# Kernel tuning notes

Measured on AMD Instinct MI355X. Metric: run time of the kernel, lower is better.

Reference implementation:

```python
import jax, jax.numpy as jnp
import numpy as np

H = 16      # num_attention_heads
D = 64      # attention_head_size
HID = H * D # hidden_size = 1024
N = 1024    # seq_len == max_len
K = 1024    # position_buckets == att_span (K >= N so un-clamped indices stay in range)
EPS = 1e-7  # layer_norm_eps


def setup_inputs() -> dict:
    key = jax.random.key(0)
    ks = jax.random.split(key, 12)

    def w(k, shape):
        return jax.random.normal(k, shape, dtype=jnp.float32) * 0.02

    return {
        "hidden_states": jax.random.normal(ks[0], (1, N, HID), dtype=jnp.float32),
        "rel_embeddings": jax.random.normal(ks[1], (2 * K, HID), dtype=jnp.float32),
        "Wq": w(ks[2], (HID, HID)), "bq": jnp.zeros((HID,), jnp.float32),
        "Wk": w(ks[3], (HID, HID)), "bk": jnp.zeros((HID,), jnp.float32),
        "Wv": w(ks[4], (HID, HID)), "bv": jnp.zeros((HID,), jnp.float32),
        "Wpk": w(ks[5], (HID, HID)), "bpk": jnp.zeros((HID,), jnp.float32),
        "Wpq": w(ks[6], (HID, HID)), "bpq": jnp.zeros((HID,), jnp.float32),
        "Wo": w(ks[7], (HID, HID)), "bo": jnp.zeros((HID,), jnp.float32),
        "ln_g": jnp.ones((HID,), jnp.float32),
        "ln_b": jnp.zeros((HID,), jnp.float32),
    }


def _heads(x):
    # (L, HID) -> (H, L, D)   (batch size is 1, matching the baked-in id offsets)
    L = x.shape[0]
    return x.reshape(L, H, D).transpose(1, 0, 2)


def reference(hidden_states, rel_embeddings, Wq, bq, Wk, bk, Wv, bv,
              Wpk, bpk, Wpq, bpq, Wo, bo, ln_g, ln_b):
    hs = hidden_states[0]                       # (N, HID)
    q = _heads(hs @ Wq.T + bq)                  # (H, N, D)
    k = _heads(hs @ Wk.T + bk)                  # (H, N, D)
    v = _heads(hs @ Wv.T + bv)                  # (H, N, D)

    scale = jnp.sqrt(jnp.asarray(D * 3, jnp.float32))  # scale_factor = 1 + c2p + p2c = 3
    scores = jnp.einsum('hid,hjd->hij', q, k) / scale  # (H, N, N)

    pos_k = _heads(rel_embeddings @ Wpk.T + bpk)       # (H, 2K, D)
    pos_q = _heads(rel_embeddings @ Wpq.T + bpq)       # (H, 2K, D)

    rows = jnp.arange(N)[:, None]                      # (N, 1)
    # ids[i, j] = (i - j) + K  (no clamp in the original; valid since K >= N)
    idx = K + jnp.arange(N)[:, None] - jnp.arange(N)[None, :]  # (N, N)

    # c2p: gather c2p_att[h, i, K + i - j]
    c2p_att = jnp.einsum('hid,hkd->hik', q, pos_k)     # (H, N, 2K)
    c2p = c2p_att[:, rows, idx]                        # (H, N, N)

    # p2c: gather p2c_att[h, i, K + j - i], then transpose last two dims
    p2c_att = jnp.einsum('hid,hkd->hik', k, pos_q)     # (H, N, 2K)
    p2c = jnp.swapaxes(p2c_att[:, rows, idx.T], -1, -2)  # (H, N, N)

    scores = scores + (c2p + p2c) / scale
    attn = jax.nn.softmax(scores, axis=-1)             # (H, N, N)

    ctx = jnp.einsum('hij,hjd->hid', attn, v)          # (H, N, D)
    ctx = ctx.transpose(1, 0, 2).reshape(1, N, HID)    # (1, N, HID)

    # DebertaV2SelfOutput: dense + residual LayerNorm
    out = ctx @ Wo.T + bo
    x = out + hidden_states
    mu = jnp.mean(x, axis=-1, keepdims=True)
    var = jnp.mean(jnp.square(x - mu), axis=-1, keepdims=True)
    return ((x - mu) / jnp.sqrt(var + EPS)) * ln_g + ln_b
```

## Files before the change

### kernel.cpp

```cpp
#include <hip/hip_runtime.h>
#include <stdint.h>

#define HID 1024
#define NSEQ 1024
#define KREL 1024
#define NHEAD 16
#define DHEAD 64

typedef __attribute__((ext_vector_type(8))) short bhalf8;
typedef __attribute__((ext_vector_type(4))) float floatx4;

__device__ inline uint16_t f2bf(float f) {
  union { float f; uint32_t u; } c; c.f = f;
  uint32_t u = c.u;
  return (uint16_t)((u + 0x7fffu + ((u >> 16) & 1u)) >> 16);
}
__device__ inline uint32_t pkbf(float a, float b) {
  union { float f; uint32_t u; } x, y; x.f = a; y.f = b;
#if __has_builtin(__builtin_amdgcn_perm)
  return __builtin_amdgcn_perm(x.u + 0x8000u, y.u + 0x8000u, 0x03020706u);
#else
  return ((x.u + 0x8000u) >> 16) | ((y.u + 0x8000u) & 0xffff0000u);
#endif
}

struct Cast8 {
  const float* src[8];
  uint16_t* dst[8];
  int n[8];
};
__global__ __launch_bounds__(256) void cast8_kernel(Cast8 c) {
  int seg = blockIdx.y;
  int n = c.n[seg];
  const float* s = c.src[seg];
  uint16_t* d = c.dst[seg];
  for (int idx = (blockIdx.x * 256 + threadIdx.x) * 4; idx < n; idx += 1024 * 256 * 4) {
    float4 v = *(const float4*)(s + idx);
    ushort4 o;
    o.x = f2bf(v.x); o.y = f2bf(v.y); o.z = f2bf(v.z); o.w = f2bf(v.w);
    *(ushort4*)(d + idx) = o;
  }
}

struct ProjArgs {
  const uint16_t* A[5];
  const uint16_t* W[5];
  const float* bias[5];
  uint16_t* C[5];
  int trans[5];
};
__global__ __launch_bounds__(256) void proj_gemm(ProjArgs pa) {
  __shared__ uint16_t a_s[2][128 * 40];
  __shared__ uint16_t b_s[2][128 * 40];
  int bidx = blockIdx.x;
  int xcd = bidx & 7, idx = bidx >> 3;
  int g = xcd * 7 + (idx >> 3);
  int nt = idx & 7;
  int z, mt;
  if (g < 24) { z = g >> 3; mt = g & 7; }
  else { int g2 = g - 24; z = 3 + (g2 >> 4); mt = g2 & 15; }
  const uint16_t* A = pa.A[z];
  const uint16_t* W = pa.W[z];
  int i0 = mt * 128, n0 = nt * 128;

  int t = threadIdx.x;
  int lane = t & 63, w = t >> 6;
  int fm = lane & 15, kq = lane >> 4;
  int wm = (w >> 1) * 64, wn = (w & 1) * 64;

  int ra = t >> 1, ca = (t & 1) * 16;
  const uint16_t* Ap = A + (size_t)(i0 + ra) * HID + ca;
  const uint16_t* Wp = W + (size_t)(n0 + ra) * HID + ca;

  floatx4 acc[4][4] = {};

  uint4 ua0 = *(const uint4*)(Ap);
  uint4 ua1 = *(const uint4*)(Ap + 8);
  uint4 ub0 = *(const uint4*)(Wp);
  uint4 ub1 = *(const uint4*)(Wp + 8);
  *(uint4*)(&a_s[0][ra * 40 + ca]) = ua0;
  *(uint4*)(&a_s[0][ra * 40 + ca + 8]) = ua1;
  *(uint4*)(&b_s[0][ra * 40 + ca]) = ub0;
  *(uint4*)(&b_s[0][ra * 40 + ca + 8]) = ub1;

  for (int kt = 0; kt < 32; ++kt) {
    __syncthreads();
    int cur = kt & 1;
    if (kt < 31) {
      int ko = (kt + 1) * 32;
      ua0 = *(const uint4*)(Ap + ko);
      ua1 = *(const uint4*)(Ap + ko + 8);
      ub0 = *(const uint4*)(Wp + ko);
      ub1 = *(const uint4*)(Wp + ko + 8);
    }
    const uint16_t* as = &a_s[cur][0];
    const uint16_t* bs = &b_s[cur][0];
    bhalf8 af[4], bf[4];
#pragma unroll
    for (int m2 = 0; m2 < 4; ++m2)
      af[m2] = *(bhalf8*)(as + (wm + m2 * 16 + fm) * 40 + kq * 8);
#pragma unroll
    for (int n2 = 0; n2 < 4; ++n2)
      bf[n2] = *(bhalf8*)(bs + (wn + n2 * 16 + fm) * 40 + kq * 8);
#pragma unroll
    for (int m2 = 0; m2 < 4; ++m2)
#pragma unroll
      for (int n2 = 0; n2 < 4; ++n2)
        acc[m2][n2] = __builtin_amdgcn_mfma_f32_16x16x32_bf16(af[m2], bf[n2], acc[m2][n2], 0, 0, 0);
    if (kt < 31) {
      int nxt = cur ^ 1;
      *(uint4*)(&a_s[nxt][ra * 40 + ca]) = ua0;
      *(uint4*)(&a_s[nxt][ra * 40 + ca + 8]) = ua1;
      *(uint4*)(&b_s[nxt][ra * 40 + ca]) = ub0;
      *(uint4*)(&b_s[nxt][ra * 40 + ca + 8]) = ub1;
    }
  }

  const float* bias = pa.bias[z];
  uint16_t* C = pa.C[z];
  int tr = pa.trans[z];
#pragma unroll
  for (int m2 = 0; m2 < 4; ++m2) {
    int rowb = i0 + wm + m2 * 16 + kq * 4;
#pragma unroll
    for (int n2 = 0; n2 < 4; ++n2) {
      int col = n0 + wn + n2 * 16 + fm;
      float bv = bias[col];
      floatx4 v = acc[m2][n2];
      if (tr) {
        uint2 p = { pkbf(v[0] + bv, v[1] + bv), pkbf(v[2] + bv, v[3] + bv) };
        *(uint2*)(C + (size_t)col * NSEQ + rowb) = p;
      } else {
#pragma unroll
        for (int r = 0; r < 4; ++r)
          C[(size_t)(rowb + r) * HID + col] = f2bf(v[r] + bv);
      }
    }
  }
}

__global__ __launch_bounds__(256) void out_gemm(const uint16_t* __restrict__ Abf,
                                                const uint16_t* __restrict__ W,
                                                const float* __restrict__ bias,
                                                float* __restrict__ C) {
  __shared__ uint16_t a_s[2][64 * 40];
  __shared__ uint16_t b_s[2][64 * 40];
  int bidx = blockIdx.x;
  int i0 = (bidx >> 4) * 64, n0 = (bidx & 15) * 64;
  int t = threadIdx.x;
  int lane = t & 63, w = t >> 6;
  int fm = lane & 15, kq = lane >> 4;
  int wm = (w >> 1) * 32, wn = (w & 1) * 32;
  int ra = t >> 2, ca = (t & 3) * 8;
  const uint16_t* Ap = Abf + (size_t)(i0 + ra) * HID + ca;
  const uint16_t* Wp = W + (size_t)(n0 + ra) * HID + ca;
  floatx4 acc00 = {0,0,0,0}, acc01 = {0,0,0,0}, acc10 = {0,0,0,0}, acc11 = {0,0,0,0};
  uint4 ua = *(const uint4*)(Ap);
  uint4 ub = *(const uint4*)(Wp);
  *(uint4*)(&a_s[0][ra * 40 + ca]) = ua;
  *(uint4*)(&b_s[0][ra * 40 + ca]) = ub;
  for (int kt = 0; kt < 32; ++kt) {
    __syncthreads();
    int cur = kt & 1;
    if (kt < 31) {
      int ko = (kt + 1) * 32;
      ua = *(const uint4*)(Ap + ko);
      ub = *(const uint4*)(Wp + ko);
    }
    const uint16_t* as = &a_s[cur][0];
    const uint16_t* bs = &b_s[cur][0];
    bhalf8 a0 = *(bhalf8*)(as + (wm + fm) * 40 + kq * 8);
    bhalf8 a1 = *(bhalf8*)(as + (wm + 16 + fm) * 40 + kq * 8);
    bhalf8 b0 = *(bhalf8*)(bs + (wn + fm) * 40 + kq * 8);
    bhalf8 b1 = *(bhalf8*)(bs + (wn + 16 + fm) * 40 + kq * 8);
    acc00 = __builtin_amdgcn_mfma_f32_16x16x32_bf16(a0, b0, acc00, 0, 0, 0);
    acc01 = __builtin_amdgcn_mfma_f32_16x16x32_bf16(a0, b1, acc01, 0, 0, 0);
    acc10 = __builtin_amdgcn_mfma_f32_16x16x32_bf16(a1, b0, acc10, 0, 0, 0);
    acc11 = __builtin_amdgcn_mfma_f32_16x16x32_bf16(a1, b1, acc11, 0, 0, 0);
    if (kt < 31) {
      int nxt = cur ^ 1;
      *(uint4*)(&a_s[nxt][ra * 40 + ca]) = ua;
      *(uint4*)(&b_s[nxt][ra * 40 + ca]) = ub;
    }
  }
  int rb0 = kq * 4;
#define EPO(ACC, SM, SN)                                                   \
  {                                                                        \
    int rowb = i0 + wm + (SM)*16 + rb0;                                    \
    int col = n0 + wn + (SN)*16 + fm;                                      \
    float bv_ = bias[col];                                                 \
    _Pragma("unroll")                                                      \
    for (int rr = 0; rr < 4; ++rr)                                         \
      C[(size_t)(rowb + rr) * HID + col] = ACC[rr] + bv_;                  \
  }
  EPO(acc00, 0, 0) EPO(acc01, 0, 1) EPO(acc10, 1, 0) EPO(acc11, 1, 1)
#undef EPO
}

__global__ __launch_bounds__(256) void attn_kernel(const uint16_t* __restrict__ qg,
                                                   const uint16_t* __restrict__ kg,
                                                   const uint16_t* __restrict__ vtg,
                                                   const uint16_t* __restrict__ pkg,
                                                   const uint16_t* __restrict__ pqg,
                                                   uint16_t* __restrict__ ctx) {
  const float RSCALE = 0.07216878364870323f;
  __shared__ uint16_t Qs[32][72];
  __shared__ uint16_t Ks[32][72];
  __shared__ uint16_t Vt[64][40];
  __shared__ uint16_t PKw[64][72];
  __shared__ uint16_t PQw[64][72];
  __shared__ float C2P[32][68];
  __shared__ float P2C[32][68];
  __shared__ float Sqk[32][36];
  __shared__ uint16_t Pbf[32][40];
  __shared__ float m_sm[32], l_sm[32], al_sm[32];

  int t = threadIdx.x;
  int lane = t & 63, w = t >> 6;
  int fm = lane & 15;
  int kq = lane >> 4;

  int b = blockIdx.x;
  int xcd = b & 7, slot = b >> 3;
  int h = xcd * 2 + (slot & 1);
  int i0 = (slot >> 1) * 32;
  int cb = h * DHEAD;

  {
    int r = t >> 3, chq = (t & 7) * 8;
    *(uint4*)(&Qs[r][chq]) = *(const uint4*)(qg + (size_t)(i0 + r) * HID + cb + chq);
  }
  if (t < 32) { m_sm[t] = -1e30f; l_sm[t] = 0.f; }

  floatx4 opv0 = {0,0,0,0}, opv1 = {0,0,0,0};
  int wn = w * 16;
  int smt = w >> 1, snt = w & 1;
  int i2 = t >> 3, jj = t & 7;

  int pr = t >> 3, pch = (t & 7) * 8;
  int rV = t >> 2, cV = (t & 3) * 8;
  const uint16_t* kb = kg + cb + pch;
  const uint16_t* vb = vtg + (size_t)(cb + rV) * HID + cV;
  const uint16_t* pkb = pkg + cb + pch;
  const uint16_t* pqb = pqg + cb + pch;

  uint4 rk, rv, rpk0, rpk1, rpq0, rpq1;
  {
    int rbase0 = KREL + i0 - 31;
    rk = *(const uint4*)(kb);
    rv = *(const uint4*)(vb);
    int rg0 = rbase0 + pr;
    int rg1 = rbase0 + pr + 32; if (rg1 > 2047) rg1 = 2047;
    rpk0 = *(const uint4*)(pkb + (size_t)rg0 * HID);
    rpk1 = *(const uint4*)(pkb + (size_t)rg1 * HID);
    rpq0 = *(const uint4*)(pqb + (size_t)rg0 * HID);
    rpq1 = *(const uint4*)(pqb + (size_t)rg1 * HID);
  }

  for (int jt = 0; jt < NSEQ / 32; ++jt) {
    int rbase = KREL + i0 - jt * 32 - 31;
    __syncthreads();
    {
      int prow = (rbase + pr) & 63;
      *(uint4*)(&Ks[pr][pch]) = rk;
      *(uint4*)(&Vt[rV][cV]) = rv;
      *(uint4*)(&PKw[prow][pch]) = rpk0;
      *(uint4*)(&PQw[prow][pch]) = rpq0;
      if (jt == 0) {
        *(uint4*)(&PKw[(prow + 32) & 63][pch]) = rpk1;
        *(uint4*)(&PQw[(prow + 32) & 63][pch]) = rpq1;
      }
    }
    __syncthreads();

    if (jt + 1 < NSEQ / 32) {
      int j0 = (jt + 1) * 32;
      int rbn = KREL + i0 - j0 - 31;
      rk = *(const uint4*)(kb + (size_t)(j0 + pr) * HID);
      rv = *(const uint4*)(vb + j0);
      rpk0 = *(const uint4*)(pkb + (size_t)(rbn + pr) * HID);
      rpq0 = *(const uint4*)(pqb + (size_t)(rbn + pr) * HID);
    }

    {
      const uint16_t* Asrc = (w < 2) ? &Qs[0][0] : &Ks[0][0];
      const uint16_t* Bsrc = (w < 2) ? &PKw[0][0] : &PQw[0][0];
      float* Cdst = (w < 2) ? &C2P[0][0] : &P2C[0][0];
      int ntb = (w & 1) * 2;
#pragma unroll
      for (int mt = 0; mt < 2; ++mt) {
        bhalf8 a0 = *(bhalf8*)(Asrc + (mt * 16 + fm) * 72 + kq * 8);
        bhalf8 a1 = *(bhalf8*)(Asrc + (mt * 16 + fm) * 72 + kq * 8 + 32);
#pragma unroll
        for (int nt = ntb; nt < ntb + 2; ++nt) {
          int wrow = (rbase + nt * 16 + fm) & 63;
          bhalf8 b0 = *(bhalf8*)(Bsrc + wrow * 72 + kq * 8);
          bhalf8 b1 = *(bhalf8*)(Bsrc + wrow * 72 + kq * 8 + 32);
          floatx4 acc = {0,0,0,0};
          acc = __builtin_amdgcn_mfma_f32_16x16x32_bf16(a0, b0, acc, 0, 0, 0);
          acc = __builtin_amdgcn_mfma_f32_16x16x32_bf16(a1, b1, acc, 0, 0, 0);
#pragma unroll
          for (int r = 0; r < 4; ++r)
            Cdst[(mt * 16 + kq * 4 + r) * 68 + nt * 16 + fm] = acc[r];
        }
      }
      bhalf8 qa0 = *(bhalf8*)(&Qs[smt * 16 + fm][kq * 8]);
      bhalf8 qa1 = *(bhalf8*)(&Qs[smt * 16 + fm][kq * 8 + 32]);
      bhalf8 kb0 = *(bhalf8*)(&Ks[snt * 16 + fm][kq * 8]);
      bhalf8 kb1 = *(bhalf8*)(&Ks[snt * 16 + fm][kq * 8 + 32]);
      floatx4 sacc = {0,0,0,0};
      sacc = __builtin_amdgcn_mfma_f32_16x16x32_bf16(qa0, kb0, sacc, 0, 0, 0);
      sacc = __builtin_amdgcn_mfma_f32_16x16x32_bf16(qa1, kb1, sacc, 0, 0, 0);
#pragma unroll
      for (int r = 0; r < 4; ++r)
        Sqk[smt * 16 + kq * 4 + r][snt * 16 + fm] = sacc[r];
    }
    __syncthreads();

    {
      float sv[4];
#pragma unroll
      for (int q = 0; q < 4; ++q) {
        int j = jj + 8 * q;
        int rr = i2 - j + 31;
        sv[q] = (Sqk[i2][j] + C2P[i2][rr] + P2C[j][rr]) * RSCALE;
      }
      float mx = fmaxf(fmaxf(sv[0], sv[1]), fmaxf(sv[2], sv[3]));
      mx = fmaxf(mx, __shfl_xor(mx, 1));
      mx = fmaxf(mx, __shfl_xor(mx, 2));
      mx = fmaxf(mx, __shfl_xor(mx, 4));
      float m_old = m_sm[i2];
      float m_new = fmaxf(m_old, mx);
      float al = __expf(m_old - m_new);
      float ts = 0.f;
#pragma unroll
      for (int q = 0; q < 4; ++q) {
        float e = __expf(sv[q] - m_new);
        Pbf[i2][jj + 8 * q] = f2bf(e);
        ts += e;
      }
      ts += __shfl_xor(ts, 1);
      ts += __shfl_xor(ts, 2);
      ts += __shfl_xor(ts, 4);
      if (jj == 0) { m_sm[i2] = m_new; l_sm[i2] = l_sm[i2] * al + ts; al_sm[i2] = al; }
    }
    __syncthreads();

    {
#pragma unroll
      for (int r = 0; r < 4; ++r) {
        opv0[r] *= al_sm[kq * 4 + r];
        opv1[r] *= al_sm[16 + kq * 4 + r];
      }
      bhalf8 vbf = *(bhalf8*)(&Vt[wn + fm][kq * 8]);
      bhalf8 pa0 = *(bhalf8*)(&Pbf[fm][kq * 8]);
      bhalf8 pa1 = *(bhalf8*)(&Pbf[16 + fm][kq * 8]);
      opv0 = __builtin_amdgcn_mfma_f32_16x16x32_bf16(pa0, vbf, opv0, 0, 0, 0);
      opv1 = __builtin_amdgcn_mfma_f32_16x16x32_bf16(pa1, vbf, opv1, 0, 0, 0);
    }
  }

#pragma unroll
  for (int r = 0; r < 4; ++r) {
    int ia = kq * 4 + r, ib = 16 + kq * 4 + r;
    float la = 1.0f / l_sm[ia], lb = 1.0f / l_sm[ib];
    ctx[(size_t)(i0 + ia) * HID + cb + wn + fm] = f2bf(opv0[r] * la);
    ctx[(size_t)(i0 + ib) * HID + cb + wn + fm] = f2bf(opv1[r] * lb);
  }
}

__global__ __launch_bounds__(256) void ln_kernel(const float* __restrict__ xin,
                                                 const float* __restrict__ hs,
                                                 const float* __restrict__ g,
                                                 const float* __restrict__ b,
                                                 float* __restrict__ y) {
  int row = blockIdx.x, t = threadIdx.x;
  int c = t * 4;
  float4 a = *(const float4*)(xin + (size_t)row * HID + c);
  float4 hv = *(const float4*)(hs + (size_t)row * HID + c);
  float x0 = a.x + hv.x, x1 = a.y + hv.y, x2 = a.z + hv.z, x3 = a.w + hv.w;
  float s = x0 + x1 + x2 + x3;
  float sq = x0 * x0 + x1 * x1 + x2 * x2 + x3 * x3;
  for (int off = 32; off; off >>= 1) {
    s += __shfl_xor(s, off);
    sq += __shfl_xor(sq, off);
  }
  __shared__ float rs[4], rq[4];
  int w = t >> 6, lane = t & 63;
  if (lane == 0) { rs[w] = s; rq[w] = sq; }
  __syncthreads();
  s = rs[0] + rs[1] + rs[2] + rs[3];
  sq = rq[0] + rq[1] + rq[2] + rq[3];
  float mu = s * (1.0f / HID);
  float var = sq * (1.0f / HID) - mu * mu;
  float rstd = rsqrtf(var + 1e-7f);
  float4 gg = *(const float4*)(g + c);
  float4 bb = *(const float4*)(b + c);
  float4 out;
  out.x = (x0 - mu) * rstd * gg.x + bb.x;
  out.y = (x1 - mu) * rstd * gg.y + bb.y;
  out.z = (x2 - mu) * rstd * gg.z + bb.z;
  out.w = (x3 - mu) * rstd * gg.w + bb.w;
  *(float4*)(y + (size_t)row * HID + c) = out;
}

extern "C" void kernel_launch(void* const* d_in, const int* in_sizes, int n_in,
                              void* d_out, int out_size, void* d_ws, size_t ws_size,
                              hipStream_t stream) {
  const float* hs  = (const float*)d_in[0];
  const float* rel = (const float*)d_in[1];
  const float* Wq  = (const float*)d_in[2];  const float* bq  = (const float*)d_in[3];
  const float* Wk  = (const float*)d_in[4];  const float* bk  = (const float*)d_in[5];
  const float* Wv  = (const float*)d_in[6];  const float* bv  = (const float*)d_in[7];
  const float* Wpk = (const float*)d_in[8];  const float* bpk = (const float*)d_in[9];
  const float* Wpq = (const float*)d_in[10]; const float* bpq = (const float*)d_in[11];
  const float* Wo  = (const float*)d_in[12]; const float* bo  = (const float*)d_in[13];
  const float* lng = (const float*)d_in[14]; const float* lnb = (const float*)d_in[15];

  char* ws = (char*)d_ws;
  const size_t MB = 1024 * 1024;
  uint16_t* q_bf   = (uint16_t*)(ws + 0 * MB);
  uint16_t* k_bf   = (uint16_t*)(ws + 2 * MB);
  uint16_t* vt_bf  = (uint16_t*)(ws + 4 * MB);
  uint16_t* pk_bf  = (uint16_t*)(ws + 6 * MB);
  uint16_t* pq_bf  = (uint16_t*)(ws + 10 * MB);
  uint16_t* ctx_bf = (uint16_t*)(ws + 14 * MB);
  float*    out_f  = (float*)   (ws + 16 * MB);
  uint16_t* hs_bf  = (uint16_t*)(ws + 20 * MB);
  uint16_t* rel_bf = (uint16_t*)(ws + 22 * MB);
  uint16_t* Wq_bf  = (uint16_t*)(ws + 26 * MB);
  uint16_t* Wk_bf  = (uint16_t*)(ws + 28 * MB);
  uint16_t* Wv_bf  = (uint16_t*)(ws + 30 * MB);
  uint16_t* Wpk_bf = (uint16_t*)(ws + 32 * MB);
  uint16_t* Wpq_bf = (uint16_t*)(ws + 34 * MB);
  uint16_t* Wo_bf  = (uint16_t*)(ws + 36 * MB);

  dim3 blk(256);

  Cast8 c8;
  c8.src[0] = hs;  c8.dst[0] = hs_bf;  c8.n[0] = 1024 * 1024;
  c8.src[1] = rel; c8.dst[1] = rel_bf; c8.n[1] = 2048 * 1024;
  c8.src[2] = Wq;  c8.dst[2] = Wq_bf;  c8.n[2] = 1024 * 1024;
  c8.src[3] = Wk;  c8.dst[3] = Wk_bf;  c8.n[3] = 1024 * 1024;
  c8.src[4] = Wv;  c8.dst[4] = Wv_bf;  c8.n[4] = 1024 * 1024;
  c8.src[5] = Wpk; c8.dst[5] = Wpk_bf; c8.n[5] = 1024 * 1024;
  c8.src[6] = Wpq; c8.dst[6] = Wpq_bf; c8.n[6] = 1024 * 1024;
  c8.src[7] = Wo;  c8.dst[7] = Wo_bf;  c8.n[7] = 1024 * 1024;
  cast8_kernel<<<dim3(1024, 8), blk, 0, stream>>>(c8);

  ProjArgs pa;
  pa.A[0] = hs_bf;  pa.A[1] = hs_bf;  pa.A[2] = hs_bf;  pa.A[3] = rel_bf; pa.A[4] = rel_bf;
  pa.W[0] = Wq_bf;  pa.W[1] = Wk_bf;  pa.W[2] = Wv_bf;  pa.W[3] = Wpk_bf; pa.W[4] = Wpq_bf;
  pa.bias[0] = bq;  pa.bias[1] = bk;  pa.bias[2] = bv;  pa.bias[3] = bpk; pa.bias[4] = bpq;
  pa.C[0] = q_bf; pa.C[1] = k_bf; pa.C[2] = vt_bf; pa.C[3] = pk_bf; pa.C[4] = pq_bf;
  pa.trans[0] = 0; pa.trans[1] = 0; pa.trans[2] = 1; pa.trans[3] = 0; pa.trans[4] = 0;
  proj_gemm<<<dim3(448), blk, 0, stream>>>(pa);

  attn_kernel<<<dim3(512), blk, 0, stream>>>(q_bf, k_bf, vt_bf, pk_bf, pq_bf, ctx_bf);

  out_gemm<<<dim3(256), blk, 0, stream>>>(ctx_bf, Wo_bf, bo, out_f);

  ln_kernel<<<dim3(1024), blk, 0, stream>>>(out_f, hs, lng, lnb, (float*)d_out);
}
```

Baseline: 201.4 us.

## Fuse fp32-to-bf16 casts into GEMM loads and keep Q fragments in registers

Removes the separate cast kernel and has the projection and output GEMMs load fp32 inputs and weights directly, converting to bf16 before the shared-memory store. This drops one launch and the write and re-read of about 9M bf16 elements, but each GEMM block now reads fp32 data from global memory, doubling its load bytes (reuse across tiles happens through cache). The attention kernel also holds its Q tile in registers instead of a shared-memory array and adds a launch-bounds occupancy hint of 3 blocks per CU.

```diff
diff --git a/kernel.cpp b/kernel.cpp
--- a/kernel.cpp
+++ b/kernel.cpp
@@ -14,6 +14,9 @@
   union { float f; uint32_t u; } c; c.f = f;
   uint32_t u = c.u;
   return (uint16_t)((u + 0x7fffu + ((u >> 16) & 1u)) >> 16);
+}
+__device__ inline uint32_t pk2(float a, float b) {
+  return (uint32_t)f2bf(a) | ((uint32_t)f2bf(b) << 16);
 }
 __device__ inline uint32_t pkbf(float a, float b) {
   union { float f; uint32_t u; } x, y; x.f = a; y.f = b;
@@ -24,27 +27,9 @@
 #endif
 }
 
-struct Cast8 {
-  const float* src[8];
-  uint16_t* dst[8];
-  int n[8];
-};
-__global__ __launch_bounds__(256) void cast8_kernel(Cast8 c) {
-  int seg = blockIdx.y;
-  int n = c.n[seg];
-  const float* s = c.src[seg];
-  uint16_t* d = c.dst[seg];
-  for (int idx = (blockIdx.x * 256 + threadIdx.x) * 4; idx < n; idx += 1024 * 256 * 4) {
-    float4 v = *(const float4*)(s + idx);
-    ushort4 o;
-    o.x = f2bf(v.x); o.y = f2bf(v.y); o.z = f2bf(v.z); o.w = f2bf(v.w);
-    *(ushort4*)(d + idx) = o;
-  }
-}
-
 struct ProjArgs {
-  const uint16_t* A[5];
-  const uint16_t* W[5];
+  const float* A[5];
+  const float* W[5];
   const float* bias[5];
   uint16_t* C[5];
   int trans[5];
@@ -59,8 +44,8 @@
   int z, mt;
   if (g < 24) { z = g >> 3; mt = g & 7; }
   else { int g2 = g - 24; z = 3 + (g2 >> 4); mt = g2 & 15; }
-  const uint16_t* A = pa.A[z];
-  const uint16_t* W = pa.W[z];
+  const float* A = pa.A[z];
+  const float* W = pa.W[z];
   int i0 = mt * 128, n0 = nt * 128;
 
   int t = threadIdx.x;
@@ -69,29 +54,38 @@
   int wm = (w >> 1) * 64, wn = (w & 1) * 64;
 
   int ra = t >> 1, ca = (t & 1) * 16;
-  const uint16_t* Ap = A + (size_t)(i0 + ra) * HID + ca;
-  const uint16_t* Wp = W + (size_t)(n0 + ra) * HID + ca;
+  const float* Ap = A + (size_t)(i0 + ra) * HID + ca;
+  const float* Wp = W + (size_t)(n0 + ra) * HID + ca;
 
   floatx4 acc[4][4] = {};
 
-  uint4 ua0 = *(const uint4*)(Ap);
-  uint4 ua1 = *(const uint4*)(Ap + 8);
-  uint4 ub0 = *(const uint4*)(Wp);
-  uint4 ub1 = *(const uint4*)(Wp + 8);
-  *(uint4*)(&a_s[0][ra * 40 + ca]) = ua0;
-  *(uint4*)(&a_s[0][ra * 40 + ca + 8]) = ua1;
-  *(uint4*)(&b_s[0][ra * 40 + ca]) = ub0;
-  *(uint4*)(&b_s[0][ra * 40 + ca + 8]) = ub1;
+  float4 fa[4], fb[4];
+#pragma unroll
+  for (int u = 0; u < 4; ++u) {
+    fa[u] = *(const float4*)(Ap + u * 4);
+    fb[u] = *(const float4*)(Wp + u * 4);
+  }
+  {
+    uint4 ua0 = { pk2(fa[0].x, fa[0].y), pk2(fa[0].z, fa[0].w), pk2(fa[1].x, fa[1].y), pk2(fa[1].z, fa[1].w) };
+    uint4 ua1 = { pk2(fa[2].x, fa[2].y), pk2(fa[2].z, fa[2].w), pk2(fa[3].x, fa[3].y), pk2(fa[3].z, fa[3].w) };
+    uint4 ub0 = { pk2(fb[0].x, fb[0].y), pk2(fb[0].z, fb[0].w), pk2(fb[1].x, fb[1].y), pk2(fb[1].z, fb[1].w) };
+    uint4 ub1 = { pk2(fb[2].x, fb[2].y), pk2(fb[2].z, fb[2].w), pk2(fb[3].x, fb[3].y), pk2(fb[3].z, fb[3].w) };
+    *(uint4*)(&a_s[0][ra * 40 + ca]) = ua0;
+    *(uint4*)(&a_s[0][ra * 40 + ca + 8]) = ua1;
+    *(uint4*)(&b_s[0][ra * 40 + ca]) = ub0;
+    *(uint4*)(&b_s[0][ra * 40 + ca + 8]) = ub1;
+  }
 
   for (int kt = 0; kt < 32; ++kt) {
     __syncthreads();
     int cur = kt & 1;
     if (kt < 31) {
       int ko = (kt + 1) * 32;
-      ua0 = *(const uint4*)(Ap + ko);
-      ua1 = *(const uint4*)(Ap + ko + 8);
-      ub0 = *(const uint4*)(Wp + ko);
-      ub1 = *(const uint4*)(Wp + ko + 8);
+#pragma unroll
+      for (int u = 0; u < 4; ++u) {
+        fa[u] = *(const float4*)(Ap + ko + u * 4);
+        fb[u] = *(const float4*)(Wp + ko + u * 4);
+      }
     }
     const uint16_t* as = &a_s[cur][0];
     const uint16_t* bs = &b_s[cur][0];
@@ -109,6 +103,10 @@
         acc[m2][n2] = __builtin_amdgcn_mfma_f32_16x16x32_bf16(af[m2], bf[n2], acc[m2][n2], 0, 0, 0);
     if (kt < 31) {
       int nxt = cur ^ 1;
+      uint4 ua0 = { pk2(fa[0].x, fa[0].y), pk2(fa[0].z, fa[0].w), pk2(fa[1].x, fa[1].y), pk2(fa[1].z, fa[1].w) };
+      uint4 ua1 = { pk2(fa[2].x, fa[2].y), pk2(fa[2].z, fa[2].w), pk2(fa[3].x, fa[3].y), pk2(fa[3].z, fa[3].w) };
+      uint4 ub0 = { pk2(fb[0].x, fb[0].y), pk2(fb[0].z, fb[0].w), pk2(fb[1].x, fb[1].y), pk2(fb[1].z, fb[1].w) };
+      uint4 ub1 = { pk2(fb[2].x, fb[2].y), pk2(fb[2].z, fb[2].w), pk2(fb[3].x, fb[3].y), pk2(fb[3].z, fb[3].w) };
       *(uint4*)(&a_s[nxt][ra * 40 + ca]) = ua0;
       *(uint4*)(&a_s[nxt][ra * 40 + ca + 8]) = ua1;
       *(uint4*)(&b_s[nxt][ra * 40 + ca]) = ub0;
@@ -140,7 +138,7 @@
 }
 
 __global__ __launch_bounds__(256) void out_gemm(const uint16_t* __restrict__ Abf,
-                                                const uint16_t* __restrict__ W,
+                                                const float* __restrict__ W,
                                                 const float* __restrict__ bias,
                                                 float* __restrict__ C) {
   __shared__ uint16_t a_s[2][64 * 40];
@@ -153,19 +151,24 @@
   int wm = (w >> 1) * 32, wn = (w & 1) * 32;
   int ra = t >> 2, ca = (t & 3) * 8;
   const uint16_t* Ap = Abf + (size_t)(i0 + ra) * HID + ca;
-  const uint16_t* Wp = W + (size_t)(n0 + ra) * HID + ca;
+  const float* Wp = W + (size_t)(n0 + ra) * HID + ca;
   floatx4 acc00 = {0,0,0,0}, acc01 = {0,0,0,0}, acc10 = {0,0,0,0}, acc11 = {0,0,0,0};
   uint4 ua = *(const uint4*)(Ap);
-  uint4 ub = *(const uint4*)(Wp);
+  float4 fw0 = *(const float4*)(Wp);
+  float4 fw1 = *(const float4*)(Wp + 4);
   *(uint4*)(&a_s[0][ra * 40 + ca]) = ua;
-  *(uint4*)(&b_s[0][ra * 40 + ca]) = ub;
+  {
+    uint4 ub = { pk2(fw0.x, fw0.y), pk2(fw0.z, fw0.w), pk2(fw1.x, fw1.y), pk2(fw1.z, fw1.w) };
+    *(uint4*)(&b_s[0][ra * 40 + ca]) = ub;
+  }
   for (int kt = 0; kt < 32; ++kt) {
     __syncthreads();
     int cur = kt & 1;
     if (kt < 31) {
       int ko = (kt + 1) * 32;
       ua = *(const uint4*)(Ap + ko);
-      ub = *(const uint4*)(Wp + ko);
+      fw0 = *(const float4*)(Wp + ko);
+      fw1 = *(const float4*)(Wp + ko + 4);
     }
     const uint16_t* as = &a_s[cur][0];
     const uint16_t* bs = &b_s[cur][0];
@@ -180,6 +183,7 @@
     if (kt < 31) {
       int nxt = cur ^ 1;
       *(uint4*)(&a_s[nxt][ra * 40 + ca]) = ua;
+      uint4 ub = { pk2(fw0.x, fw0.y), pk2(fw0.z, fw0.w), pk2(fw1.x, fw1.y), pk2(fw1.z, fw1.w) };
       *(uint4*)(&b_s[nxt][ra * 40 + ca]) = ub;
     }
   }
@@ -197,14 +201,13 @@
 #undef EPO
 }
 
-__global__ __launch_bounds__(256) void attn_kernel(const uint16_t* __restrict__ qg,
-                                                   const uint16_t* __restrict__ kg,
-                                                   const uint16_t* __restrict__ vtg,
-                                                   const uint16_t* __restrict__ pkg,
-                                                   const uint16_t* __restrict__ pqg,
-                                                   uint16_t* __restrict__ ctx) {
+__global__ __launch_bounds__(256, 3) void attn_kernel(const uint16_t* __restrict__ qg,
+                                                      const uint16_t* __restrict__ kg,
+                                                      const uint16_t* __restrict__ vtg,
+                                                      const uint16_t* __restrict__ pkg,
+                                                      const uint16_t* __restrict__ pqg,
+                                                      uint16_t* __restrict__ ctx) {
   const float RSCALE = 0.07216878364870323f;
-  __shared__ uint16_t Qs[32][72];
   __shared__ uint16_t Ks[32][72];
   __shared__ uint16_t Vt[64][40];
   __shared__ uint16_t PKw[64][72];
@@ -226,10 +229,13 @@
   int i0 = (slot >> 1) * 32;
   int cb = h * DHEAD;
 
-  {
-    int r = t >> 3, chq = (t & 7) * 8;
-    *(uint4*)(&Qs[r][chq]) = *(const uint4*)(qg + (size_t)(i0 + r) * HID + cb + chq);
-  }
+  bhalf8 qreg[2][2];
+#pragma unroll
+  for (int mt = 0; mt < 2; ++mt)
+#pragma unroll
+    for (int h8 = 0; h8 < 2; ++h8)
+      qreg[mt][h8] = *(const bhalf8*)(qg + (size_t)(i0 + mt * 16 + fm) * HID + cb + kq * 8 + h8 * 32);
+
   if (t < 32) { m_sm[t] = -1e30f; l_sm[t] = 0.f; }
 
   floatx4 opv0 = {0,0,0,0}, opv1 = {0,0,0,0};
@@ -283,14 +289,19 @@
     }
 
     {
-      const uint16_t* Asrc = (w < 2) ? &Qs[0][0] : &Ks[0][0];
       const uint16_t* Bsrc = (w < 2) ? &PKw[0][0] : &PQw[0][0];
       float* Cdst = (w < 2) ? &C2P[0][0] : &P2C[0][0];
       int ntb = (w & 1) * 2;
 #pragma unroll
       for (int mt = 0; mt < 2; ++mt) {
-        bhalf8 a0 = *(bhalf8*)(Asrc + (mt * 16 + fm) * 72 + kq * 8);
-        bhalf8 a1 = *(bhalf8*)(Asrc + (mt * 16 + fm) * 72 + kq * 8 + 32);
+        bhalf8 a0, a1;
+        if (w < 2) {
+          a0 = qreg[mt][0];
+          a1 = qreg[mt][1];
+        } else {
+          a0 = *(bhalf8*)(&Ks[mt * 16 + fm][kq * 8]);
+          a1 = *(bhalf8*)(&Ks[mt * 16 + fm][kq * 8 + 32]);
+        }
 #pragma unroll
         for (int nt = ntb; nt < ntb + 2; ++nt) {
           int wrow = (rbase + nt * 16 + fm) & 63;
@@ -304,8 +315,8 @@
             Cdst[(mt * 16 + kq * 4 + r) * 68 + nt * 16 + fm] = acc[r];
         }
       }
-      bhalf8 qa0 = *(bhalf8*)(&Qs[smt * 16 + fm][kq * 8]);
-      bhalf8 qa1 = *(bhalf8*)(&Qs[smt * 16 + fm][kq * 8 + 32]);
+      bhalf8 qa0 = qreg[smt][0];
+      bhalf8 qa1 = qreg[smt][1];
       bhalf8 kb0 = *(bhalf8*)(&Ks[snt * 16 + fm][kq * 8]);
       bhalf8 kb1 = *(bhalf8*)(&Ks[snt * 16 + fm][kq * 8 + 32]);
       floatx4 sacc = {0,0,0,0};
@@ -426,31 +437,12 @@
   uint16_t* pq_bf  = (uint16_t*)(ws + 10 * MB);
   uint16_t* ctx_bf = (uint16_t*)(ws + 14 * MB);
   float*    out_f  = (float*)   (ws + 16 * MB);
-  uint16_t* hs_bf  = (uint16_t*)(ws + 20 * MB);
-  uint16_t* rel_bf = (uint16_t*)(ws + 22 * MB);
-  uint16_t* Wq_bf  = (uint16_t*)(ws + 26 * MB);
-  uint16_t* Wk_bf  = (uint16_t*)(ws + 28 * MB);
-  uint16_t* Wv_bf  = (uint16_t*)(ws + 30 * MB);
-  uint16_t* Wpk_bf = (uint16_t*)(ws + 32 * MB);
-  uint16_t* Wpq_bf = (uint16_t*)(ws + 34 * MB);
-  uint16_t* Wo_bf  = (uint16_t*)(ws + 36 * MB);
 
   dim3 blk(256);
 
-  Cast8 c8;
-  c8.src[0] = hs;  c8.dst[0] = hs_bf;  c8.n[0] = 1024 * 1024;
-  c8.src[1] = rel; c8.dst[1] = rel_bf; c8.n[1] = 2048 * 1024;
-  c8.src[2] = Wq;  c8.dst[2] = Wq_bf;  c8.n[2] = 1024 * 1024;
-  c8.src[3] = Wk;  c8.dst[3] = Wk_bf;  c8.n[3] = 1024 * 1024;
-  c8.src[4] = Wv;  c8.dst[4] = Wv_bf;  c8.n[4] = 1024 * 1024;
-  c8.src[5] = Wpk; c8.dst[5] = Wpk_bf; c8.n[5] = 1024 * 1024;
-  c8.src[6] = Wpq; c8.dst[6] = Wpq_bf; c8.n[6] = 1024 * 1024;
-  c8.src[7] = Wo;  c8.dst[7] = Wo_bf;  c8.n[7] = 1024 * 1024;
-  cast8_kernel<<<dim3(1024, 8), blk, 0, stream>>>(c8);
-
   ProjArgs pa;
-  pa.A[0] = hs_bf;  pa.A[1] = hs_bf;  pa.A[2] = hs_bf;  pa.A[3] = rel_bf; pa.A[4] = rel_bf;
-  pa.W[0] = Wq_bf;  pa.W[1] = Wk_bf;  pa.W[2] = Wv_bf;  pa.W[3] = Wpk_bf; pa.W[4] = Wpq_bf;
+  pa.A[0] = hs;  pa.A[1] = hs;  pa.A[2] = hs;  pa.A[3] = rel; pa.A[4] = rel;
+  pa.W[0] = Wq;  pa.W[1] = Wk;  pa.W[2] = Wv;  pa.W[3] = Wpk; pa.W[4] = Wpq;
   pa.bias[0] = bq;  pa.bias[1] = bk;  pa.bias[2] = bv;  pa.bias[3] = bpk; pa.bias[4] = bpq;
   pa.C[0] = q_bf; pa.C[1] = k_bf; pa.C[2] = vt_bf; pa.C[3] = pk_bf; pa.C[4] = pq_bf;
   pa.trans[0] = 0; pa.trans[1] = 0; pa.trans[2] = 1; pa.trans[3] = 0; pa.trans[4] = 0;
@@ -458,7 +450,7 @@
 
   attn_kernel<<<dim3(512), blk, 0, stream>>>(q_bf, k_bf, vt_bf, pk_bf, pq_bf, ctx_bf);
 
-  out_gemm<<<dim3(256), blk, 0, stream>>>(ctx_bf, Wo_bf, bo, out_f);
+  out_gemm<<<dim3(256), blk, 0, stream>>>(ctx_bf, Wo, bo, out_f);
 
   ln_kernel<<<dim3(1024), blk, 0, stream>>>(out_f, hs, lng, lnb, (float*)d_out);
 }
```

Result: slower. 255.4 us (+26.8%).
